# Kernel optimization log

Hardware: AMD Instinct MI355X
Metric: run time of the kernel (lower is better)

Reference implementation:

```python
import jax, jax.numpy as jnp
import numpy as np
from jax import lax

TAU = 2.0      # membrane time constant
V_TH = 1.0     # spiking threshold
V_RESET = 0.0  # reset potential (hard reset)
ALPHA = 1.0    # PiecewiseQuadratic surrogate width parameter


@jax.custom_vjp
def spike(u):
    # Heaviside: emit spike when membrane potential exceeds threshold (u = h - v_th)
    return (u >= 0.0).astype(u.dtype)


def _spike_fwd(u):
    return spike(u), u


def _spike_bwd(u, g):
    # PiecewiseQuadratic surrogate gradient: alpha - alpha^2*|u| for |u| < 1/alpha, else 0
    sg = jnp.maximum(ALPHA - (ALPHA * ALPHA) * jnp.abs(u), 0.0)
    return (g * sg,)


spike.defvjp(_spike_fwd, _spike_bwd)


def setup_inputs() -> dict:
    key = jax.random.key(0)
    T, B, N = 64, 64, 8192
    x = jax.random.normal(key, (T, B, N), dtype=jnp.float32)
    return {"x": x}


def reference(x):
    # STBP LIF recurrence over the leading time dimension.
    #   h_t = v_{t-1} + (x_t - (v_{t-1} - v_reset)) / tau   (leaky integration)
    #   s_t = Heaviside(h_t - v_th)                          (spike, surrogate grad)
    #   v_t = h_t * (1 - s_t) + v_reset * s_t                (hard reset)
    def step(v, xt):
        h = v + (xt - (v - V_RESET)) / TAU
        s = spike(h - V_TH)
        v_new = h * (1.0 - s) + V_RESET * s
        return v_new, s

    v0 = jnp.zeros_like(x[0])
    _, spikes = lax.scan(step, v0, x)
    return spikes  # [T, B, N]
```

## Files before the change

### kernel.cpp

```cpp
#include <hip/hip_runtime.h>


constexpr int T_STEPS = 64;
constexpr int PF = 8;

typedef float f32x4 __attribute__((ext_vector_type(4)));

__global__ __launch_bounds__(256) void lif_kernel(const f32x4* __restrict__ x,
                                                  f32x4* __restrict__ out,
                                                  int cols4) {
    const int idx = blockIdx.x * blockDim.x + threadIdx.x;
    if (idx >= cols4) return;

    const f32x4* xp = x + idx;
    f32x4* op = out + idx;

    f32x4 v = {0.f, 0.f, 0.f, 0.f};
    f32x4 bufA[PF], bufB[PF];

    auto load8 = [&](f32x4 (&dst)[PF], int tbase) {
#pragma unroll
        for (int i = 0; i < PF; ++i)
            dst[i] = xp[(tbase + i) * cols4];
    };

    auto compute8 = [&](f32x4 (&cur)[PF], int tbase) {
#pragma unroll
        for (int i = 0; i < PF; ++i) {
            const f32x4 h = 0.5f * (v + cur[i]);
            f32x4 s;
            s.x = (h.x >= 1.0f) ? 1.0f : 0.0f;
            s.y = (h.y >= 1.0f) ? 1.0f : 0.0f;
            s.z = (h.z >= 1.0f) ? 1.0f : 0.0f;
            s.w = (h.w >= 1.0f) ? 1.0f : 0.0f;
            v.x = (h.x >= 1.0f) ? 0.0f : h.x;
            v.y = (h.y >= 1.0f) ? 0.0f : h.y;
            v.z = (h.z >= 1.0f) ? 0.0f : h.z;
            v.w = (h.w >= 1.0f) ? 0.0f : h.w;
            __builtin_nontemporal_store(s, &op[(tbase + i) * cols4]);
        }
    };

    load8(bufA, 0);
    load8(bufB, 8);
    compute8(bufA, 0);   load8(bufA, 16);
    compute8(bufB, 8);   load8(bufB, 24);
    compute8(bufA, 16);  load8(bufA, 32);
    compute8(bufB, 24);  load8(bufB, 40);
    compute8(bufA, 32);  load8(bufA, 48);
    compute8(bufB, 40);  load8(bufB, 56);
    compute8(bufA, 48);
    compute8(bufB, 56);
}

extern "C" void kernel_launch(void* const* d_in, const int* in_sizes, int n_in,
                              void* d_out, int out_size, void* d_ws, size_t ws_size,
                              hipStream_t stream) {
    const float* x = (const float*)d_in[0];
    float* out = (float*)d_out;

    const int total = in_sizes[0];
    const int cols = total / T_STEPS;
    const int cols4 = cols / 4;

    const int block = 256;
    const int grid = (cols4 + block - 1) / block;
    lif_kernel<<<grid, block, 0, stream>>>((const f32x4*)x, (f32x4*)out, cols4);
}
```

Before: 228.4 us.

## Stream LIF inputs through per-wave LDS double buffers via async global-to-LDS loads

Input loads now use global_load_lds, which copies each time-step chunk straight into a per-wave double-buffered LDS region instead of into register prefetch arrays. The loop waits on hand-written vmcnt counts that take the interleaved stores into account, and it reads each step from LDS. The aim is to free VGPRs and keep more loads in flight to hide memory latency in this bandwidth-bound scan. In exchange it adds LDS traffic, relies on fragile manual waitcnt accounting, and drops the bounds check on the column index.

Result: no change. 227.7 us (-0.3%).

```diff
diff --git a/kernel.cpp b/kernel.cpp
--- a/kernel.cpp
+++ b/kernel.cpp
@@ -1,33 +1,56 @@
 #include <hip/hip_runtime.h>
+#include <stdint.h>
 
 
 constexpr int T_STEPS = 64;
-constexpr int PF = 8;
+constexpr int CHUNK = 8;
+constexpr int NCHUNK = T_STEPS / CHUNK;
+constexpr int WAVES = 4;
 
 typedef float f32x4 __attribute__((ext_vector_type(4)));
+typedef __attribute__((address_space(3))) uint8_t lds_u8;
+typedef __attribute__((address_space(1))) const uint8_t glb_u8;
 
 __global__ __launch_bounds__(256) void lif_kernel(const f32x4* __restrict__ x,
                                                   f32x4* __restrict__ out,
                                                   int cols4) {
-    const int idx = blockIdx.x * blockDim.x + threadIdx.x;
-    if (idx >= cols4) return;
+    __shared__ f32x4 lds[WAVES][2][CHUNK][64];
 
-    const f32x4* xp = x + idx;
-    f32x4* op = out + idx;
+    const int tid = threadIdx.x;
+    const int w = tid >> 6;
+    const int lane = tid & 63;
+    const int col4 = blockIdx.x * 256 + tid;
+
+    const f32x4* xp = x + col4;
+    f32x4* op = out + col4;
+
+    auto issue_chunk = [&](int c, int p) {
+#pragma unroll
+        for (int r = 0; r < CHUNK; ++r) {
+            const f32x4* g = xp + (c * CHUNK + r) * cols4;
+            __builtin_amdgcn_global_load_lds((glb_u8*)g, (lds_u8*)&lds[w][p][r][0],
+                                             16, 0, 0);
+        }
+        __builtin_amdgcn_sched_barrier(0);
+    };
+
+    issue_chunk(0, 0);
+    issue_chunk(1, 1);
 
     f32x4 v = {0.f, 0.f, 0.f, 0.f};
-    f32x4 bufA[PF], bufB[PF];
 
-    auto load8 = [&](f32x4 (&dst)[PF], int tbase) {
 #pragma unroll
-        for (int i = 0; i < PF; ++i)
-            dst[i] = xp[(tbase + i) * cols4];
-    };
+    for (int c = 0; c < NCHUNK; ++c) {
+        const int p = c & 1;
+        if (c == 0 || c == NCHUNK - 1)
+            asm volatile("s_waitcnt vmcnt(8)" ::: "memory");
+        else
+            asm volatile("s_waitcnt vmcnt(16)" ::: "memory");
 
-    auto compute8 = [&](f32x4 (&cur)[PF], int tbase) {
 #pragma unroll
-        for (int i = 0; i < PF; ++i) {
-            const f32x4 h = 0.5f * (v + cur[i]);
+        for (int r = 0; r < CHUNK; ++r) {
+            const f32x4 xt = lds[w][p][r][lane];
+            const f32x4 h = 0.5f * (v + xt);
             f32x4 s;
             s.x = (h.x >= 1.0f) ? 1.0f : 0.0f;
             s.y = (h.y >= 1.0f) ? 1.0f : 0.0f;
@@ -37,20 +60,12 @@
             v.y = (h.y >= 1.0f) ? 0.0f : h.y;
             v.z = (h.z >= 1.0f) ? 0.0f : h.z;
             v.w = (h.w >= 1.0f) ? 0.0f : h.w;
-            __builtin_nontemporal_store(s, &op[(tbase + i) * cols4]);
+            __builtin_nontemporal_store(s, op + (c * CHUNK + r) * cols4);
         }
-    };
+        __builtin_amdgcn_sched_barrier(0);
 
-    load8(bufA, 0);
-    load8(bufB, 8);
-    compute8(bufA, 0);   load8(bufA, 16);
-    compute8(bufB, 8);   load8(bufB, 24);
-    compute8(bufA, 16);  load8(bufA, 32);
-    compute8(bufB, 24);  load8(bufB, 40);
-    compute8(bufA, 32);  load8(bufA, 48);
-    compute8(bufB, 40);  load8(bufB, 56);
-    compute8(bufA, 48);
-    compute8(bufB, 56);
+        if (c + 2 < NCHUNK) issue_chunk(c + 2, p);
+    }
 }
 
 extern "C" void kernel_launch(void* const* d_in, const int* in_sizes, int n_in,
```
